# Optimization experiments

Measured on AMD Instinct MI355X. Metric: run time of the kernel, lower is better.

The kernel has to match this reference:

```python
import jax, jax.numpy as jnp
import numpy as np

B, T, S, D, V = 8, 128, 400, 512, 50000
EPS_LN = 1e-6

def setup_inputs() -> dict:
    key = jax.random.key(0)
    ks = jax.random.split(key, 10)
    a = jax.random.uniform(ks[0], (B, T, S), dtype=jnp.float32)
    attn_weights = a / jnp.sum(a, axis=-1, keepdims=True)  # row-stochastic like softmax attention
    return {
        'x': jax.random.normal(ks[1], (B, T, D), dtype=jnp.float32),
        'x_t': jax.random.normal(ks[2], (B, T, D), dtype=jnp.float32),
        'memory': jax.random.normal(ks[3], (B, S, D), dtype=jnp.float32),
        'attn_weights': attn_weights,
        'src': jax.random.randint(ks[4], (B, S), 0, V),
        'norm_a': jnp.ones((D,), jnp.float32),
        'norm_b': jnp.zeros((D,), jnp.float32),
        'proj_w': jax.random.normal(ks[5], (V, D), dtype=jnp.float32) * (1.0 / np.sqrt(D)),
        'proj_b': jnp.zeros((V,), jnp.float32),
        'wh_w': jax.random.normal(ks[6], (1, D), dtype=jnp.float32) * (1.0 / np.sqrt(D)),
        'wh_b': jnp.zeros((1,), jnp.float32),
        'ws_w': jax.random.normal(ks[7], (1, D), dtype=jnp.float32) * (1.0 / np.sqrt(D)),
        'ws_b': jnp.zeros((1,), jnp.float32),
        'wx_w': jax.random.normal(ks[8], (1, D), dtype=jnp.float32) * (1.0 / np.sqrt(D)),
        'wx_b': jnp.zeros((1,), jnp.float32),
        'bptr': jnp.zeros((1, 1), jnp.float32),
    }

def _layer_norm(x, a, b):
    mu = jnp.mean(x, axis=-1, keepdims=True)
    sd = jnp.std(x, axis=-1, keepdims=True)
    return a * (x - mu) / (sd + EPS_LN) + b

def reference(x, x_t, memory, attn_weights, src, norm_a, norm_b, proj_w, proj_b,
              wh_w, wh_b, ws_w, ws_b, wx_w, wx_b, bptr):
    # generation distribution over vocab: [B,T,V]
    dec_dist = jnp.einsum('btd,vd->btv', _layer_norm(x, norm_a, norm_b), proj_w) + proj_b
    # context vector h_t = attn @ memory: [B,T,D]
    h_t = jnp.einsum('bts,bsd->btd', attn_weights, memory)
    # p_gen gate: [B,T,1]
    logits = (jnp.einsum('btd,od->bto', h_t, wh_w) + wh_b
              + jnp.einsum('btd,od->bto', x, ws_w) + ws_b
              + jnp.einsum('btd,od->bto', x_t, wx_w) + wx_b
              + bptr[0, 0])
    p_gen = jax.nn.sigmoid(logits)
    # copy distribution via scatter_add of attention mass onto source token ids
    b_idx = jnp.arange(B)[:, None, None]
    t_idx = jnp.arange(T)[None, :, None]
    v_idx = src[:, None, :]  # broadcast over T -> [B,T,S] index
    enc_attn_dist = jnp.zeros((B, T, V), dtype=dec_dist.dtype).at[b_idx, t_idx, v_idx].add(attn_weights)
    out = jnp.log(p_gen * jax.nn.softmax(dec_dist, axis=-1) + (1.0 - p_gen) * enc_attn_dist + 1e-12)
    return out, p_gen
```

## Files before the change

kernel.cpp:

```cpp
#include <hip/hip_runtime.h>
#include <hip/hip_bf16.h>
#include <cstdint>

#define B_  8
#define T_  128
#define S_  400
#define D_  512
#define V_  50000
#define M_  (B_*T_)
#define NT_ 391
#define EPS_LN 1e-6f

#define WCONV_BLKS 12500
#define MW_BLKS    (B_*S_)
#define ROWS_BLKS  M_

typedef __bf16 bf16x8 __attribute__((ext_vector_type(8)));
typedef float  f32x4  __attribute__((ext_vector_type(4)));
typedef unsigned short u16;
typedef unsigned short u16x8 __attribute__((ext_vector_type(8)));

__device__ __forceinline__ float bf2f(u16 u) {
    union { unsigned i; float f; } c; c.i = ((unsigned)u) << 16; return c.f;
}
__device__ __forceinline__ u16 f2bf(float f) {
    union { float f; unsigned i; } c; c.f = f;
    unsigned i = c.i;
    unsigned r = (i + 0x7FFFu + ((i >> 16) & 1u)) >> 16;
    return (u16)r;
}

__device__ __forceinline__ float bsum(float v, float* sb) {
    #pragma unroll
    for (int o = 32; o; o >>= 1) v += __shfl_xor(v, o);
    __syncthreads();
    if ((threadIdx.x & 63) == 0) sb[threadIdx.x >> 6] = v;
    __syncthreads();
    return sb[0] + sb[1] + sb[2] + sb[3];
}

__global__ void k_pre(const float* __restrict__ pw, u16* __restrict__ wb,
                      const float* __restrict__ mem, const float* __restrict__ whw,
                      float* __restrict__ mw,
                      const float* __restrict__ x, const float* __restrict__ xt,
                      const float* __restrict__ attn,
                      const float* __restrict__ na, const float* __restrict__ nb,
                      const float* __restrict__ wsw, const float* __restrict__ wxw,
                      const float* __restrict__ whb, const float* __restrict__ wsb,
                      const float* __restrict__ wxb, const float* __restrict__ bp,
                      u16* __restrict__ Ab, float* __restrict__ pgen,
                      float* __restrict__ outp) {
    __shared__ float sb[4];
    int bid = blockIdx.x;
    int tid = threadIdx.x;
    if (bid < WCONV_BLKS) {
        size_t i = ((size_t)bid * 256 + tid) * 8;
        float4 a = *(const float4*)(pw + i);
        float4 b = *(const float4*)(pw + i + 4);
        u16x8 o;
        o[0] = f2bf(a.x); o[1] = f2bf(a.y); o[2] = f2bf(a.z); o[3] = f2bf(a.w);
        o[4] = f2bf(b.x); o[5] = f2bf(b.y); o[6] = f2bf(b.z); o[7] = f2bf(b.w);
        *(u16x8*)(wb + i) = o;
        return;
    }
    if (bid < WCONV_BLKS + MW_BLKS) {
        int row = bid - WCONV_BLKS;
        const float* mr = mem + (size_t)row * D_;
        float2 m2 = *(const float2*)(mr + tid * 2);
        float2 w2 = *(const float2*)(whw + tid * 2);
        float tot = bsum(m2.x * w2.x + m2.y * w2.y, sb);
        if (tid == 0) mw[row] = tot;
        return;
    }
    {
        int row = bid - WCONV_BLKS - MW_BLKS;
        int b = row / T_;
        const float* xr  = x  + (size_t)row * D_;
        const float* xtr = xt + (size_t)row * D_;
        float2 xv = *(const float2*)(xr + tid * 2);
        float tsx  = bsum(xv.x + xv.y, sb);
        float tsx2 = bsum(xv.x * xv.x + xv.y * xv.y, sb);
        float mu  = tsx / (float)D_;
        float var = fmaxf(tsx2 / (float)D_ - mu * mu, 0.f);
        float rs  = 1.f / (sqrtf(var) + EPS_LN);
        float2 nav = *(const float2*)(na + tid * 2);
        float2 nbv = *(const float2*)(nb + tid * 2);
        u16 a0 = f2bf(nav.x * (xv.x - mu) * rs + nbv.x);
        u16 a1 = f2bf(nav.y * (xv.y - mu) * rs + nbv.y);
        ((unsigned*)(Ab + (size_t)row * D_))[tid] = (unsigned)a0 | ((unsigned)a1 << 16);
        float2 wsv = *(const float2*)(wsw + tid * 2);
        float2 wxv = *(const float2*)(wxw + tid * 2);
        float2 xtv = *(const float2*)(xtr + tid * 2);
        float dot = xv.x * wsv.x + xv.y * wsv.y + xtv.x * wxv.x + xtv.y * wxv.y;
        if (tid < 200) {
            const float* ar  = attn + (size_t)row * S_;
            const float* mwb = mw + b * S_;
            float2 av = *(const float2*)(ar + tid * 2);
            float2 mv = *(const float2*)(mwb + tid * 2);
            dot += av.x * mv.x + av.y * mv.y;
        }
        float tdot = bsum(dot, sb);
        if (tid == 0) {
            float logit = tdot + whb[0] + wsb[0] + wxb[0] + bp[0];
            float p = 1.f / (1.f + __expf(-logit));
            pgen[row] = p;
            outp[row] = p;
        }
    }
}

__global__ __launch_bounds__(256) void k_gemm(const u16* __restrict__ Ab,
                                              const u16* __restrict__ Wb,
                                              const float* __restrict__ projb,
                                              u16* __restrict__ dec,
                                              float* __restrict__ psum) {
    __shared__ __align__(16) char smem[49152];
    int bid = blockIdx.x;
    int xcd = bid & 7, loc = bid >> 3;
    int wg = xcd * NT_ + loc;
    int mt = wg & 7, nt = wg >> 3;
    int brow = mt * 128, bcol = nt * 128;
    int tid = threadIdx.x, lane = tid & 63, wv = tid >> 6;
    int wm = wv >> 1, wn = wv & 1;
    int kq = lane >> 4, lr = lane & 15;

    size_t aoff[2], boff[2];
    int flatoff[2];
    #pragma unroll
    for (int i = 0; i < 2; ++i) {
        int flat = i * 4096 + tid * 16;
        flatoff[i] = flat;
        int sub = flat >> 10;
        int l   = (flat >> 4) & 63;
        int kq2 = l >> 4, lr2 = l & 15;
        int arow = brow + sub * 16 + lr2;
        int vrow = bcol + sub * 16 + lr2; if (vrow >= V_) vrow = V_ - 1;
        aoff[i] = (size_t)arow * 512 + kq2 * 8;
        boff[i] = (size_t)vrow * 512 + kq2 * 8;
    }

#define STAGE(buf, kt) { \
    char* ab = smem + (buf) * 16384; \
    _Pragma("unroll") \
    for (int i = 0; i < 2; ++i) { \
        __builtin_amdgcn_global_load_lds( \
            (const __attribute__((address_space(1))) unsigned*)(Ab + aoff[i] + (size_t)(kt) * 32), \
            (__attribute__((address_space(3))) unsigned*)(ab + flatoff[i]), 16, 0, 0); \
        __builtin_amdgcn_global_load_lds( \
            (const __attribute__((address_space(1))) unsigned*)(Wb + boff[i] + (size_t)(kt) * 32), \
            (__attribute__((address_space(3))) unsigned*)(ab + 8192 + flatoff[i]), 16, 0, 0); \
    } }

    f32x4 acc[4][4] = {};
    STAGE(0, 0);
    STAGE(1, 1);
    STAGE(2, 2);
    asm volatile("s_waitcnt vmcnt(8)" ::: "memory");
    __builtin_amdgcn_s_barrier();
    __builtin_amdgcn_sched_barrier(0);
    int cur = 0;
    for (int kt = 0; kt < 16; ++kt) {
        const bf16x8* Afp = (const bf16x8*)(smem + cur * 16384);
        const bf16x8* Bfp = (const bf16x8*)(smem + cur * 16384 + 8192);
        bf16x8 af[4], bfr[4];
        #pragma unroll
        for (int m = 0; m < 4; ++m) af[m]  = Afp[(wm * 4 + m) * 64 + lane];
        #pragma unroll
        for (int n = 0; n < 4; ++n) bfr[n] = Bfp[(wn * 4 + n) * 64 + lane];
        #pragma unroll
        for (int m = 0; m < 4; ++m)
            #pragma unroll
            for (int n = 0; n < 4; ++n)
                acc[m][n] = __builtin_amdgcn_mfma_f32_16x16x32_bf16(af[m], bfr[n], acc[m][n], 0, 0, 0);
        __builtin_amdgcn_sched_barrier(0);
        if (kt == 15) break;
        if (kt < 14) { asm volatile("s_waitcnt vmcnt(4)" ::: "memory"); }
        else         { asm volatile("s_waitcnt vmcnt(0)" ::: "memory"); }
        __builtin_amdgcn_s_barrier();
        __builtin_amdgcn_sched_barrier(0);
        if (kt < 13) STAGE(cur, kt + 3);
        cur = (cur == 2) ? 0 : cur + 1;
    }
#undef STAGE
    __syncthreads();

    float pbn[4]; int cvaln[4];
    #pragma unroll
    for (int n = 0; n < 4; ++n) {
        int col = bcol + wn * 64 + n * 16 + lr;
        cvaln[n] = (col < V_);
        pbn[n] = cvaln[n] ? projb[col] : 0.f;
    }
    u16 (*Os)[136] = (u16(*)[136])smem;
    float* ssum = (float*)(smem + 34816);
    #pragma unroll
    for (int m = 0; m < 4; ++m) {
        #pragma unroll
        for (int i = 0; i < 4; ++i) {
            int row128 = wm * 64 + m * 16 + kq * 4 + i;
            float se = 0.f;
            #pragma unroll
            for (int n = 0; n < 4; ++n) {
                float dv = acc[m][n][i] + pbn[n];
                if (cvaln[n]) se += __expf(dv);
                Os[row128][wn * 64 + n * 16 + lr] = f2bf(dv);
            }
            #pragma unroll
            for (int o = 1; o < 16; o <<= 1) se += __shfl_xor(se, o);
            if (lr == 0) ssum[wn * 128 + row128] = se;
        }
    }
    __syncthreads();
    if (tid < 128) {
        psum[(size_t)(brow + tid) * NT_ + nt] = ssum[tid] + ssum[128 + tid];
    }
    #pragma unroll
    for (int j = 0; j < 8; ++j) {
        int row = j * 16 + (tid >> 4);
        int c8 = (tid & 15) * 8;
        int gcol = bcol + c8;
        if (gcol + 8 <= V_) {
            u16x8 v = *(const u16x8*)&Os[row][c8];
            *(u16x8*)(dec + (size_t)(brow + row) * V_ + gcol) = v;
        }
    }
}

__global__ void k_final(const u16* __restrict__ dec, const float* __restrict__ pgen,
                        const float* __restrict__ psum, float* __restrict__ out) {
    __shared__ float sb[4];
    int row = blockIdx.y;
    int t = threadIdx.x;
    const float* ps = psum + (size_t)row * NT_;
    float s = 0.f;
    for (int j = t; j < NT_; j += 256) s += ps[j];
    s = bsum(s, sb);
    float C = __logf(pgen[row]) - __logf(s);
    int v0 = (blockIdx.x * 256 + t) * 8;
    if (v0 >= V_) return;
    u16x8 d = *(const u16x8*)(dec + (size_t)row * V_ + v0);
    float o[8];
    bool rare = false;
    #pragma unroll
    for (int j = 0; j < 8; ++j) {
        o[j] = bf2f(d[j]) + C;
        rare |= (o[j] < -24.f);
    }
    if (__any(rare)) {
        #pragma unroll
        for (int j = 0; j < 8; ++j)
            if (o[j] < -24.f) o[j] = __logf(__expf(o[j]) + 1e-12f);
    }
    float* op = out + (size_t)row * V_ + v0;
    float4 o0, o1;
    o0.x = o[0]; o0.y = o[1]; o0.z = o[2]; o0.w = o[3];
    o1.x = o[4]; o1.y = o[5]; o1.z = o[6]; o1.w = o[7];
    *(float4*)op = o0;
    *(float4*)(op + 4) = o1;
}

__global__ void k_fix(const int* __restrict__ src, const float* __restrict__ attn,
                      const u16* __restrict__ dec, const float* __restrict__ pgen,
                      const float* __restrict__ psum, float* __restrict__ out) {
    __shared__ float sb[4];
    __shared__ int   sh_sr[S_];
    __shared__ int   sh_fs[S_];
    __shared__ float sh_enc[S_];
    int b = blockIdx.x >> 7;
    int t = blockIdx.x & 127;
    int tid = threadIdx.x;
    int row = b * T_ + t;
    const float* ps = psum + (size_t)row * NT_;
    float s = 0.f;
    for (int j = tid; j < NT_; j += 256) s += ps[j];
    s = bsum(s, sb);
    float bs = __logf(s);
    const int* sr = src + b * S_;
    for (int s2 = tid; s2 < S_; s2 += 256) { sh_sr[s2] = sr[s2]; sh_enc[s2] = 0.f; }
    __syncthreads();
    for (int s2 = tid; s2 < S_; s2 += 256) {
        int v = sh_sr[s2];
        int f = 0;
        while (sh_sr[f] != v) ++f;
        sh_fs[s2] = f;
    }
    __syncthreads();
    const float* ar = attn + (size_t)row * S_;
    for (int s2 = tid; s2 < S_; s2 += 256)
        atomicAdd(&sh_enc[sh_fs[s2]], ar[s2]);
    __syncthreads();
    float p = pgen[row];
    for (int s2 = tid; s2 < S_; s2 += 256) {
        if (sh_fs[s2] == s2) {
            int v = sh_sr[s2];
            float d = bf2f(dec[(size_t)row * V_ + v]);
            out[(size_t)row * V_ + v] =
                __logf(p * __expf(d - bs) + (1.f - p) * sh_enc[s2] + 1e-12f);
        }
    }
}

extern "C" void kernel_launch(void* const* d_in, const int* in_sizes, int n_in,
                              void* d_out, int out_size, void* d_ws, size_t ws_size,
                              hipStream_t stream) {
    const float* x    = (const float*)d_in[0];
    const float* xt   = (const float*)d_in[1];
    const float* mem  = (const float*)d_in[2];
    const float* attn = (const float*)d_in[3];
    const int*   src  = (const int*)d_in[4];
    const float* na   = (const float*)d_in[5];
    const float* nb   = (const float*)d_in[6];
    const float* pw   = (const float*)d_in[7];
    const float* pb   = (const float*)d_in[8];
    const float* whw  = (const float*)d_in[9];
    const float* whb  = (const float*)d_in[10];
    const float* wsw  = (const float*)d_in[11];
    const float* wsb  = (const float*)d_in[12];
    const float* wxw  = (const float*)d_in[13];
    const float* wxb  = (const float*)d_in[14];
    const float* bp   = (const float*)d_in[15];

    char* ws = (char*)d_ws;
    u16*   Wb   = (u16*)(ws + 0);
    u16*   Ab   = (u16*)(ws + 51200000);
    u16*   dec  = (u16*)(ws + 52248576);
    float* psum = (float*)(ws + 154648576);
    float* mw   = (float*)(ws + 156250112);
    float* pgen = (float*)(ws + 156262912);
    float* out  = (float*)d_out;
    float* outp = out + (size_t)M_ * V_;

    k_pre  <<<WCONV_BLKS + MW_BLKS + ROWS_BLKS, 256, 0, stream>>>(
               pw, Wb, mem, whw, mw, x, xt, attn, na, nb,
               wsw, wxw, whb, wsb, wxb, bp, Ab, pgen, outp);
    k_gemm <<<3128, 256, 0, stream>>>(Ab, Wb, pb, dec, psum);
    k_final<<<dim3(25, M_), 256, 0, stream>>>(dec, pgen, psum, out);
    k_fix  <<<B_ * T_, 256, 0, stream>>>(src, attn, dec, pgen, psum, out);
}
```

Measured before the change: 263.2 us.

## Merge final and fix kernels using a per-batch source-token bitmask

Builds a per-batch bitmask of source token ids in the pre-pass kernel. The final log-softmax pass and the copy-distribution fix are merged into one launch, with the fix blocks first. The bulk blocks use the bitmask to skip writing entries the fix blocks own, which removes a kernel launch and the write-after-write ordering between the two passes. Waves that touch masked words fall back to scalar stores, and every bulk block still recomputes the psum reduction.

```diff
diff --git a/kernel.cpp b/kernel.cpp
--- a/kernel.cpp
+++ b/kernel.cpp
@@ -14,6 +14,8 @@
 #define WCONV_BLKS 12500
 #define MW_BLKS    (B_*S_)
 #define ROWS_BLKS  M_
+#define BM_BLKS    B_
+#define BM_WORDS   1600
 
 typedef __bf16 bf16x8 __attribute__((ext_vector_type(8)));
 typedef float  f32x4  __attribute__((ext_vector_type(4)));
@@ -48,9 +50,11 @@
                       const float* __restrict__ wsw, const float* __restrict__ wxw,
                       const float* __restrict__ whb, const float* __restrict__ wsb,
                       const float* __restrict__ wxb, const float* __restrict__ bp,
+                      const int* __restrict__ src, unsigned* __restrict__ bm,
                       u16* __restrict__ Ab, float* __restrict__ pgen,
                       float* __restrict__ outp) {
     __shared__ float sb[4];
+    __shared__ unsigned sbm[BM_WORDS];
     int bid = blockIdx.x;
     int tid = threadIdx.x;
     if (bid < WCONV_BLKS) {
@@ -72,7 +76,7 @@
         if (tid == 0) mw[row] = tot;
         return;
     }
-    {
+    if (bid < WCONV_BLKS + MW_BLKS + ROWS_BLKS) {
         int row = bid - WCONV_BLKS - MW_BLKS;
         int b = row / T_;
         const float* xr  = x  + (size_t)row * D_;
@@ -106,6 +110,20 @@
             pgen[row] = p;
             outp[row] = p;
         }
+        return;
+    }
+    {
+        int b = bid - WCONV_BLKS - MW_BLKS - ROWS_BLKS;
+        for (int i = tid; i < BM_WORDS; i += 256) sbm[i] = 0u;
+        __syncthreads();
+        const int* sr = src + b * S_;
+        for (int s = tid; s < S_; s += 256) {
+            int v = sr[s];
+            atomicOr(&sbm[v >> 5], 1u << (v & 31));
+        }
+        __syncthreads();
+        unsigned* dst = bm + b * BM_WORDS;
+        for (int i = tid; i < BM_WORDS; i += 256) dst[i] = sbm[i];
     }
 }
 
@@ -226,77 +244,85 @@
     }
 }
 
-__global__ void k_final(const u16* __restrict__ dec, const float* __restrict__ pgen,
-                        const float* __restrict__ psum, float* __restrict__ out) {
-    __shared__ float sb[4];
-    int row = blockIdx.y;
-    int t = threadIdx.x;
-    const float* ps = psum + (size_t)row * NT_;
-    float s = 0.f;
-    for (int j = t; j < NT_; j += 256) s += ps[j];
-    s = bsum(s, sb);
-    float C = __logf(pgen[row]) - __logf(s);
-    int v0 = (blockIdx.x * 256 + t) * 8;
-    if (v0 >= V_) return;
-    u16x8 d = *(const u16x8*)(dec + (size_t)row * V_ + v0);
-    float o[8];
-    bool rare = false;
-    #pragma unroll
-    for (int j = 0; j < 8; ++j) {
-        o[j] = bf2f(d[j]) + C;
-        rare |= (o[j] < -24.f);
-    }
-    if (__any(rare)) {
-        #pragma unroll
-        for (int j = 0; j < 8; ++j)
-            if (o[j] < -24.f) o[j] = __logf(__expf(o[j]) + 1e-12f);
-    }
-    float* op = out + (size_t)row * V_ + v0;
-    float4 o0, o1;
-    o0.x = o[0]; o0.y = o[1]; o0.z = o[2]; o0.w = o[3];
-    o1.x = o[4]; o1.y = o[5]; o1.z = o[6]; o1.w = o[7];
-    *(float4*)op = o0;
-    *(float4*)(op + 4) = o1;
-}
-
-__global__ void k_fix(const int* __restrict__ src, const float* __restrict__ attn,
-                      const u16* __restrict__ dec, const float* __restrict__ pgen,
-                      const float* __restrict__ psum, float* __restrict__ out) {
+__global__ void k_post(const u16* __restrict__ dec, const float* __restrict__ pgen,
+                       const float* __restrict__ psum, const unsigned* __restrict__ bm,
+                       const int* __restrict__ src, const float* __restrict__ attn,
+                       float* __restrict__ out) {
     __shared__ float sb[4];
     __shared__ int   sh_sr[S_];
     __shared__ int   sh_fs[S_];
     __shared__ float sh_enc[S_];
-    int b = blockIdx.x >> 7;
-    int t = blockIdx.x & 127;
+    int bid = blockIdx.x;
     int tid = threadIdx.x;
-    int row = b * T_ + t;
+    if (bid < M_) {
+        int b = bid >> 7;
+        int row = bid;
+        const float* ps = psum + (size_t)row * NT_;
+        float s = 0.f;
+        for (int j = tid; j < NT_; j += 256) s += ps[j];
+        s = bsum(s, sb);
+        float bs = __logf(s);
+        const int* sr = src + b * S_;
+        for (int s2 = tid; s2 < S_; s2 += 256) { sh_sr[s2] = sr[s2]; sh_enc[s2] = 0.f; }
+        __syncthreads();
+        for (int s2 = tid; s2 < S_; s2 += 256) {
+            int v = sh_sr[s2];
+            int f = 0;
+            while (sh_sr[f] != v) ++f;
+            sh_fs[s2] = f;
+        }
+        __syncthreads();
+        const float* ar = attn + (size_t)row * S_;
+        for (int s2 = tid; s2 < S_; s2 += 256)
+            atomicAdd(&sh_enc[sh_fs[s2]], ar[s2]);
+        __syncthreads();
+        float p = pgen[row];
+        for (int s2 = tid; s2 < S_; s2 += 256) {
+            if (sh_fs[s2] == s2) {
+                int v = sh_sr[s2];
+                float d = bf2f(dec[(size_t)row * V_ + v]);
+                out[(size_t)row * V_ + v] =
+                    __logf(p * __expf(d - bs) + (1.f - p) * sh_enc[s2] + 1e-12f);
+            }
+        }
+        return;
+    }
+    int fid = bid - M_;
+    int c = fid % 25, row = fid / 25;
+    int b = row >> 7;
     const float* ps = psum + (size_t)row * NT_;
     float s = 0.f;
     for (int j = tid; j < NT_; j += 256) s += ps[j];
     s = bsum(s, sb);
-    float bs = __logf(s);
-    const int* sr = src + b * S_;
-    for (int s2 = tid; s2 < S_; s2 += 256) { sh_sr[s2] = sr[s2]; sh_enc[s2] = 0.f; }
-    __syncthreads();
-    for (int s2 = tid; s2 < S_; s2 += 256) {
-        int v = sh_sr[s2];
-        int f = 0;
-        while (sh_sr[f] != v) ++f;
-        sh_fs[s2] = f;
-    }
-    __syncthreads();
-    const float* ar = attn + (size_t)row * S_;
-    for (int s2 = tid; s2 < S_; s2 += 256)
-        atomicAdd(&sh_enc[sh_fs[s2]], ar[s2]);
-    __syncthreads();
-    float p = pgen[row];
-    for (int s2 = tid; s2 < S_; s2 += 256) {
-        if (sh_fs[s2] == s2) {
-            int v = sh_sr[s2];
-            float d = bf2f(dec[(size_t)row * V_ + v]);
-            out[(size_t)row * V_ + v] =
-                __logf(p * __expf(d - bs) + (1.f - p) * sh_enc[s2] + 1e-12f);
-        }
+    float C = __logf(pgen[row]) - __logf(s);
+    int v0 = c * 2048 + tid * 8;
+    if (v0 >= V_) return;
+    unsigned w = bm[b * BM_WORDS + (v0 >> 5)];
+    unsigned mask = (w >> ((tid & 3) * 8)) & 0xFFu;
+    u16x8 d = *(const u16x8*)(dec + (size_t)row * V_ + v0);
+    float o[8];
+    bool rare = false;
+    #pragma unroll
+    for (int j = 0; j < 8; ++j) {
+        o[j] = bf2f(d[j]) + C;
+        rare |= (o[j] < -24.f);
+    }
+    if (__any(rare)) {
+        #pragma unroll
+        for (int j = 0; j < 8; ++j)
+            if (o[j] < -24.f) o[j] = __logf(__expf(o[j]) + 1e-12f);
+    }
+    float* op = out + (size_t)row * V_ + v0;
+    if (__any(mask != 0)) {
+        #pragma unroll
+        for (int j = 0; j < 8; ++j)
+            if (!((mask >> j) & 1u)) op[j] = o[j];
+    } else {
+        float4 o0, o1;
+        o0.x = o[0]; o0.y = o[1]; o0.z = o[2]; o0.w = o[3];
+        o1.x = o[4]; o1.y = o[5]; o1.z = o[6]; o1.w = o[7];
+        *(float4*)op = o0;
+        *(float4*)(op + 4) = o1;
     }
 }
 
@@ -321,19 +347,19 @@
     const float* bp   = (const float*)d_in[15];
 
     char* ws = (char*)d_ws;
-    u16*   Wb   = (u16*)(ws + 0);
-    u16*   Ab   = (u16*)(ws + 51200000);
-    u16*   dec  = (u16*)(ws + 52248576);
-    float* psum = (float*)(ws + 154648576);
-    float* mw   = (float*)(ws + 156250112);
-    float* pgen = (float*)(ws + 156262912);
+    u16*     Wb   = (u16*)(ws + 0);
+    u16*     Ab   = (u16*)(ws + 51200000);
+    u16*     dec  = (u16*)(ws + 52248576);
+    float*   psum = (float*)(ws + 154648576);
+    float*   mw   = (float*)(ws + 156250112);
+    float*   pgen = (float*)(ws + 156262912);
+    unsigned* bmp = (unsigned*)(ws + 156267008);
     float* out  = (float*)d_out;
     float* outp = out + (size_t)M_ * V_;
 
-    k_pre  <<<WCONV_BLKS + MW_BLKS + ROWS_BLKS, 256, 0, stream>>>(
-               pw, Wb, mem, whw, mw, x, xt, attn, na, nb,
-               wsw, wxw, whb, wsb, wxb, bp, Ab, pgen, outp);
-    k_gemm <<<3128, 256, 0, stream>>>(Ab, Wb, pb, dec, psum);
-    k_final<<<dim3(25, M_), 256, 0, stream>>>(dec, pgen, psum, out);
-    k_fix  <<<B_ * T_, 256, 0, stream>>>(src, attn, dec, pgen, psum, out);
-}
+    k_pre <<<WCONV_BLKS + MW_BLKS + ROWS_BLKS + BM_BLKS, 256, 0, stream>>>(
+              pw, Wb, mem, whw, mw, x, xt, attn, na, nb,
+              wsw, wxw, whb, wsb, wxb, bp, src, bmp, Ab, pgen, outp);
+    k_gemm<<<3128, 256, 0, stream>>>(Ab, Wb, pb, dec, psum);
+    k_post<<<M_ + 25 * M_, 256, 0, stream>>>(dec, pgen, psum, bmp, src, attn, out);
+}
```

Result: slower. 285.4 us, median of 2 (+8.4%).
